# Optimization experiments

Measured on AMD Instinct MI355X. Metric: run time of the kernel, lower is better.

Reference implementation:

```python
import jax, jax.numpy as jnp
import numpy as np

N = 8192      # number of nodes
D = 256       # embedding dim
K = 32        # k_degree
EPS = 1e-6


def setup_inputs() -> dict:
    key = jax.random.key(0)
    k1, k2 = jax.random.split(key)
    x = jax.random.normal(k1, (N, D), dtype=jnp.float32)
    q = jax.random.uniform(k2, (N, N), dtype=jnp.float32)  # gumbel uniform noise
    temperature = jnp.array([0.001], dtype=jnp.float32)    # learned nn.Parameter
    return {"x": x, "q": q, "temperature": temperature}


def reference(x, q, temperature):
    # torch: dist_mat = sum(x - x.unsqueeze(1), dim=-1) ** 2
    # dist_mat[i, j] = (sum_f x[j,f] - sum_f x[i,f])^2 = (s[j] - s[i])^2
    s = jnp.sum(x, axis=-1)                      # [N]
    dist_mat = (s[None, :] - s[:, None]) ** 2    # [N, N]
    probs = jnp.exp(-temperature[0] * dist_mat) + EPS

    # Gumbel-perturbed logits, top-k per column via argsort along axis 0
    g = jnp.log(probs + EPS) - jnp.log(-jnp.log(q + EPS))  # [N, N]
    child_nodes = jnp.argsort(g, axis=0)[-K:].reshape(-1)   # [K*N]
    parent_nodes = jnp.tile(jnp.arange(N, dtype=child_nodes.dtype), K)  # [K*N]

    # symmetric scatter of adjacency mask
    mask = jnp.zeros((N, N), dtype=x.dtype)
    mask = mask.at[child_nodes, parent_nodes].set(1.0)
    mask = mask.at[parent_nodes, child_nodes].set(1.0)

    edge_index = jnp.stack([child_nodes, parent_nodes])      # [2, K*N]
    edge_weights = jnp.ones((edge_index.shape[1],), dtype=x.dtype)
    return edge_index, edge_weights, probs, mask, dist_mat
```

## Files before the change

### kernel.cpp

```cpp
#include <hip/hip_runtime.h>
#include <stdint.h>

typedef unsigned long long ull;
#define NN 8192
#define KK 32

__device__ __forceinline__ ull make_key(float g, int idx) {
    uint32_t b = __float_as_uint(g);
    uint32_t k = b ^ (0x80000000u | (uint32_t)((int32_t)b >> 31));
    return ((ull)k << 32) | (uint32_t)idx;
}

__device__ __forceinline__ void cas_both(ull &a, ull &b) {
    ull x = a, y = b;
    bool g = x < y;
    a = g ? y : x;
    b = g ? x : y;
}

__device__ __forceinline__ void sort16_desc(ull (&c)[16]) {
#pragma unroll
    for (int k = 2; k <= 16; k <<= 1) {
#pragma unroll
        for (int j = k >> 1; j > 0; j >>= 1) {
#pragma unroll
            for (int i = 0; i < 16; ++i) {
                int l = i ^ j;
                if (l > i) {
                    if ((i & k) == 0) cas_both(c[i], c[l]);
                    else              cas_both(c[l], c[i]);
                }
            }
        }
    }
}

__device__ __forceinline__ void bmerge32_desc(ull (&c)[32]) {
#pragma unroll
    for (int j = 16; j > 0; j >>= 1) {
#pragma unroll
        for (int i = 0; i < 32; ++i) {
            if ((i & j) == 0) cas_both(c[i], c[i ^ j]);
        }
    }
}

__device__ __forceinline__ void merge_into32(ull (&acc)[32], const ull (&ch)[32]) {
#pragma unroll
    for (int k = 0; k < 32; ++k) {
        ull a = acc[31 - k], b = ch[k];
        acc[31 - k] = a >= b ? a : b;
    }
    bmerge32_desc(acc);
}

__device__ __forceinline__ void load_list32(const ull* __restrict__ src, int list,
                                            int j, ull (&ch)[32]) {
#pragma unroll
    for (int k = 0; k < 32; ++k)
        ch[k] = src[((size_t)list * 32 + k) * NN + j];
}

__global__ __launch_bounds__(256) void k_rowsum(const float* __restrict__ x,
                                                float* __restrict__ s) {
    int row  = blockIdx.x * 4 + (threadIdx.x >> 6);
    int lane = threadIdx.x & 63;
    float4 v = reinterpret_cast<const float4*>(x)[(size_t)row * 64 + lane];
    float sum = (v.x + v.y) + (v.z + v.w);
#pragma unroll
    for (int off = 1; off < 64; off <<= 1) sum += __shfl_xor(sum, off, 64);
    if (lane == 0) s[row] = sum;
}

__global__ __launch_bounds__(256, 2) void k_fused(const float* __restrict__ q,
                                                  const float* __restrict__ s,
                                                  const float* __restrict__ tptr,
                                                  float* __restrict__ dist_out,
                                                  float* __restrict__ probs_out,
                                                  ull* __restrict__ cand,
                                                  int segr) {
    const int j = blockIdx.x * 256 + threadIdx.x;
    const float sj = s[j];
    const float temp = tptr[0];

    ull top[32];
#pragma unroll
    for (int k = 0; k < 32; ++k) top[k] = 0;

    const int i0 = blockIdx.y * segr;
    for (int r = 0; r < segr; r += 16) {
        float qv[16];
#pragma unroll
        for (int u = 0; u < 16; ++u)
            qv[u] = q[(size_t)(i0 + r + u) * NN + j];

        ull ch[16];
#pragma unroll
        for (int u = 0; u < 16; ++u) {
            const int i = i0 + r + u;
            float diff = sj - s[i];
            float d = diff * diff;
            float pr = expf(-(temp * d)) + 1e-6f;
            size_t off = (size_t)i * NN + j;
            dist_out[off]  = d;
            probs_out[off] = pr;
            float a = logf(pr + 1e-6f);
            float b = logf(-logf(qv[u] + 1e-6f));
            ch[u] = make_key(a - b, i);
        }
        sort16_desc(ch);
#pragma unroll
        for (int u = 0; u < 16; ++u) {
            ull a = top[16 + u], b = ch[15 - u];
            top[16 + u] = a >= b ? a : b;
        }
        bmerge32_desc(top);
    }
    const size_t base = (size_t)blockIdx.y * KK * NN + j;
#pragma unroll
    for (int k = 0; k < KK; ++k) cand[base + (size_t)k * NN] = top[k];
}

__global__ __launch_bounds__(256) void k_merge1(const ull* __restrict__ src,
                                                ull* __restrict__ dst) {
    int gid = blockIdx.x * 256 + threadIdx.x;
    int j   = gid & (NN - 1);
    int grp = gid >> 13;
    ull acc[32];
    load_list32(src, grp * 4, j, acc);
#pragma unroll
    for (int l = 1; l < 4; ++l) {
        ull ch[32];
        load_list32(src, grp * 4 + l, j, ch);
        merge_into32(acc, ch);
    }
    const size_t base = (size_t)grp * KK * NN + j;
#pragma unroll
    for (int k = 0; k < KK; ++k) dst[base + (size_t)k * NN] = acc[k];
}

__global__ __launch_bounds__(256) void k_final(const ull* __restrict__ src,
                                               float* __restrict__ out) {
    const int j = blockIdx.x * 256 + threadIdx.x;
    ull acc[32];
    load_list32(src, 0, j, acc);
#pragma unroll
    for (int l = 1; l < 4; ++l) {
        ull ch[32];
        load_list32(src, l, j, ch);
        merge_into32(acc, ch);
    }
    const size_t KN = (size_t)KK * NN;
    float* child  = out;
    float* parent = out + KN;
    float* wts    = out + 2 * KN;
    float* mask   = out + 3 * KN + (size_t)NN * NN;
#pragma unroll
    for (int k = 0; k < KK; ++k) {
        uint32_t c = (uint32_t)acc[KK - 1 - k];
        child [(size_t)k * NN + j] = (float)c;
        parent[(size_t)k * NN + j] = (float)j;
        wts   [(size_t)k * NN + j] = 1.0f;
        mask[(size_t)c * NN + j] = 1.0f;
        mask[(size_t)j * NN + c] = 1.0f;
    }
}

extern "C" void kernel_launch(void* const* d_in, const int* in_sizes, int n_in,
                              void* d_out, int out_size, void* d_ws, size_t ws_size,
                              hipStream_t stream) {
    const float* x    = (const float*)d_in[0];
    const float* q    = (const float*)d_in[1];
    const float* tptr = (const float*)d_in[2];
    float* out = (float*)d_out;

    const size_t KN = (size_t)KK * NN;
    float* probs_out = out + 3 * KN;
    float* mask_out  = out + 3 * KN + (size_t)NN * NN;
    float* dist_out  = out + 3 * KN + 2 * (size_t)NN * NN;

    const int nseg = 16;
    const int segr = NN / nseg;
    float* s = (float*)d_ws;
    ull* cand0 = (ull*)((char*)d_ws + 65536);
    ull* cand1 = cand0 + (size_t)NN * nseg * KK;

    k_rowsum<<<NN / 4, 256, 0, stream>>>(x, s);
    k_fused<<<dim3(NN / 256, nseg), 256, 0, stream>>>(q, s, tptr, dist_out,
                                                      probs_out, cand0, segr);
    (void)hipMemsetAsync(mask_out, 0, (size_t)NN * NN * sizeof(float), stream);
    k_merge1<<<(NN * 4) / 256, 256, 0, stream>>>(cand0, cand1);
    k_final<<<NN / 256, 256, 0, stream>>>(cand1, out);
}
```

Measured before the change: 386.6 us.

## Fuse mask zeroing into main kernel, use more segments, merge top-k in one tail

The separate memset of the NN×NN mask is removed. Each thread of the fused kernel now zeroes a strided slice of the mask with nontemporal float4 stores while it computes dist/probs. The row dimension is split into 32 segments instead of 16, using 8-row batches and a target occupancy of 4. The two merge kernels become a single tail kernel that merges all segment lists serially per column. Loads and stores for streaming data are marked nontemporal. The single tail kernel runs far fewer threads and merges 32 lists one after another, which risks a latency-bound tail, and the smaller batches add more merge work per row.

Measured after the change: 461.9 us. 1.19x slower.

```diff
diff --git a/kernel.cpp b/kernel.cpp
--- a/kernel.cpp
+++ b/kernel.cpp
@@ -2,6 +2,7 @@
 #include <stdint.h>
 
 typedef unsigned long long ull;
+typedef float __attribute__((ext_vector_type(4))) floatx4;
 #define NN 8192
 #define KK 32
 
@@ -18,13 +19,14 @@
     b = g ? x : y;
 }
 
-__device__ __forceinline__ void sort16_desc(ull (&c)[16]) {
+template <int SZ>
+__device__ __forceinline__ void sortN_desc(ull (&c)[SZ]) {
 #pragma unroll
-    for (int k = 2; k <= 16; k <<= 1) {
+    for (int k = 2; k <= SZ; k <<= 1) {
 #pragma unroll
         for (int j = k >> 1; j > 0; j >>= 1) {
 #pragma unroll
-            for (int i = 0; i < 16; ++i) {
+            for (int i = 0; i < SZ; ++i) {
                 int l = i ^ j;
                 if (l > i) {
                     if ((i & k) == 0) cas_both(c[i], c[l]);
@@ -54,13 +56,6 @@
     bmerge32_desc(acc);
 }
 
-__device__ __forceinline__ void load_list32(const ull* __restrict__ src, int list,
-                                            int j, ull (&ch)[32]) {
-#pragma unroll
-    for (int k = 0; k < 32; ++k)
-        ch[k] = src[((size_t)list * 32 + k) * NN + j];
-}
-
 __global__ __launch_bounds__(256) void k_rowsum(const float* __restrict__ x,
                                                 float* __restrict__ s) {
     int row  = blockIdx.x * 4 + (threadIdx.x >> 6);
@@ -72,89 +67,86 @@
     if (lane == 0) s[row] = sum;
 }
 
-__global__ __launch_bounds__(256, 2) void k_fused(const float* __restrict__ q,
+__global__ __launch_bounds__(256, 4) void k_fused(const float* __restrict__ q,
                                                   const float* __restrict__ s,
                                                   const float* __restrict__ tptr,
                                                   float* __restrict__ dist_out,
                                                   float* __restrict__ probs_out,
+                                                  floatx4* __restrict__ mask4,
                                                   ull* __restrict__ cand,
-                                                  int segr) {
+                                                  int segr, int nthreads) {
     const int j = blockIdx.x * 256 + threadIdx.x;
+    const int gtid = (blockIdx.y * (NN / 256) + blockIdx.x) * 256 + threadIdx.x;
     const float sj = s[j];
     const float temp = tptr[0];
+    const floatx4 z4 = {0.f, 0.f, 0.f, 0.f};
 
     ull top[32];
 #pragma unroll
     for (int k = 0; k < 32; ++k) top[k] = 0;
 
     const int i0 = blockIdx.y * segr;
-    for (int r = 0; r < segr; r += 16) {
-        float qv[16];
+    for (int r = 0; r < segr; r += 8) {
+        const int it = r >> 3;
+        float qv[8];
 #pragma unroll
-        for (int u = 0; u < 16; ++u)
-            qv[u] = q[(size_t)(i0 + r + u) * NN + j];
+        for (int u = 0; u < 8; ++u)
+            qv[u] = __builtin_nontemporal_load(&q[(size_t)(i0 + r + u) * NN + j]);
 
-        ull ch[16];
+        ull ch[8];
 #pragma unroll
-        for (int u = 0; u < 16; ++u) {
+        for (int u = 0; u < 8; ++u) {
             const int i = i0 + r + u;
             float diff = sj - s[i];
             float d = diff * diff;
             float pr = expf(-(temp * d)) + 1e-6f;
             size_t off = (size_t)i * NN + j;
-            dist_out[off]  = d;
-            probs_out[off] = pr;
+            __builtin_nontemporal_store(d, &dist_out[off]);
+            __builtin_nontemporal_store(pr, &probs_out[off]);
             float a = logf(pr + 1e-6f);
             float b = logf(-logf(qv[u] + 1e-6f));
             ch[u] = make_key(a - b, i);
         }
-        sort16_desc(ch);
 #pragma unroll
-        for (int u = 0; u < 16; ++u) {
-            ull a = top[16 + u], b = ch[15 - u];
-            top[16 + u] = a >= b ? a : b;
+        for (int u = 0; u < 2; ++u)
+            __builtin_nontemporal_store(
+                z4, &mask4[(size_t)(it * 2 + u) * nthreads + gtid]);
+
+        sortN_desc<8>(ch);
+#pragma unroll
+        for (int u = 0; u < 8; ++u) {
+            ull a = top[24 + u], b = ch[7 - u];
+            top[24 + u] = a >= b ? a : b;
         }
         bmerge32_desc(top);
     }
     const size_t base = (size_t)blockIdx.y * KK * NN + j;
 #pragma unroll
-    for (int k = 0; k < KK; ++k) cand[base + (size_t)k * NN] = top[k];
+    for (int k = 0; k < KK; ++k)
+        __builtin_nontemporal_store(top[k], &cand[base + (size_t)k * NN]);
 }
 
-__global__ __launch_bounds__(256) void k_merge1(const ull* __restrict__ src,
-                                                ull* __restrict__ dst) {
-    int gid = blockIdx.x * 256 + threadIdx.x;
-    int j   = gid & (NN - 1);
-    int grp = gid >> 13;
+__global__ __launch_bounds__(64) void k_tail(const ull* __restrict__ src,
+                                             float* __restrict__ out,
+                                             float* __restrict__ mask,
+                                             int nlists) {
+    const int j = blockIdx.x * 64 + threadIdx.x;
     ull acc[32];
-    load_list32(src, grp * 4, j, acc);
 #pragma unroll
-    for (int l = 1; l < 4; ++l) {
+    for (int k = 0; k < 32; ++k)
+        acc[k] = __builtin_nontemporal_load(&src[(size_t)k * NN + j]);
+    for (int l = 1; l < nlists; ++l) {
         ull ch[32];
-        load_list32(src, grp * 4 + l, j, ch);
-        merge_into32(acc, ch);
-    }
-    const size_t base = (size_t)grp * KK * NN + j;
 #pragma unroll
-    for (int k = 0; k < KK; ++k) dst[base + (size_t)k * NN] = acc[k];
-}
-
-__global__ __launch_bounds__(256) void k_final(const ull* __restrict__ src,
-                                               float* __restrict__ out) {
-    const int j = blockIdx.x * 256 + threadIdx.x;
-    ull acc[32];
-    load_list32(src, 0, j, acc);
-#pragma unroll
-    for (int l = 1; l < 4; ++l) {
-        ull ch[32];
-        load_list32(src, l, j, ch);
+        for (int k = 0; k < 32; ++k)
+            ch[k] = __builtin_nontemporal_load(
+                &src[((size_t)l * 32 + k) * NN + j]);
         merge_into32(acc, ch);
     }
     const size_t KN = (size_t)KK * NN;
     float* child  = out;
     float* parent = out + KN;
     float* wts    = out + 2 * KN;
-    float* mask   = out + 3 * KN + (size_t)NN * NN;
 #pragma unroll
     for (int k = 0; k < KK; ++k) {
         uint32_t c = (uint32_t)acc[KK - 1 - k];
@@ -179,16 +171,16 @@
     float* mask_out  = out + 3 * KN + (size_t)NN * NN;
     float* dist_out  = out + 3 * KN + 2 * (size_t)NN * NN;
 
-    const int nseg = 16;
+    int nseg = 32;
+    if (ws_size < 65536 + (size_t)NN * 32 * KK * 8) nseg = 16;
     const int segr = NN / nseg;
+    const int nthreads = (NN / 256) * nseg * 256;
     float* s = (float*)d_ws;
     ull* cand0 = (ull*)((char*)d_ws + 65536);
-    ull* cand1 = cand0 + (size_t)NN * nseg * KK;
 
     k_rowsum<<<NN / 4, 256, 0, stream>>>(x, s);
-    k_fused<<<dim3(NN / 256, nseg), 256, 0, stream>>>(q, s, tptr, dist_out,
-                                                      probs_out, cand0, segr);
-    (void)hipMemsetAsync(mask_out, 0, (size_t)NN * NN * sizeof(float), stream);
-    k_merge1<<<(NN * 4) / 256, 256, 0, stream>>>(cand0, cand1);
-    k_final<<<NN / 256, 256, 0, stream>>>(cand1, out);
+    k_fused<<<dim3(NN / 256, nseg), 256, 0, stream>>>(
+        q, s, tptr, dist_out, probs_out, (floatx4*)mask_out, cand0, segr,
+        nthreads);
+    k_tail<<<NN / 64, 64, 0, stream>>>(cand0, out, mask_out, nseg);
 }
```
